# Performance work log

Measured on AMD Instinct MI355X. Metric: run time of the kernel, lower is better.

## Reference

```python
import jax, jax.numpy as jnp
import numpy as np

N_NODES = 50000
N_EDGES = 800000
IN_CH, HID_CH, OUT_CH = 128, 256, 128


def _glorot(key, shape):
    fan_in, fan_out = shape[1], shape[0]
    lim = float(np.sqrt(6.0 / (fan_in + fan_out)))
    return jax.random.uniform(key, shape, jnp.float32, -lim, lim)


def setup_inputs() -> dict:
    key = jax.random.key(0)
    ks = jax.random.split(key, 8)
    x = jax.random.normal(ks[0], (N_NODES, IN_CH), jnp.float32)
    edge_index = jax.random.randint(ks[1], (2, N_EDGES), 0, N_NODES, jnp.int64)
    return {
        "x": x,
        "edge_index": edge_index,
        # layer 1: SAGEConv(128 -> 256): lin_l (with bias) on aggregated, lin_r (no bias) on root
        "W1l": _glorot(ks[2], (HID_CH, IN_CH)),
        "b1l": jnp.zeros((HID_CH,), jnp.float32),
        "W1r": _glorot(ks[3], (HID_CH, IN_CH)),
        # layer 2: SAGEConv(256 -> 128)
        "W2l": _glorot(ks[4], (OUT_CH, HID_CH)),
        "b2l": jnp.zeros((OUT_CH,), jnp.float32),
        "W2r": _glorot(ks[5], (OUT_CH, HID_CH)),
    }


def _sage_conv(x, src, dst, Wl, bl, Wr, n_nodes):
    # mean-aggregate neighbor (source) features at destination nodes
    msg = x[src]                                                   # [E, C] gather
    agg = jax.ops.segment_sum(msg, dst, num_segments=n_nodes)      # [N, C]
    deg = jax.ops.segment_sum(jnp.ones((src.shape[0],), x.dtype), dst,
                              num_segments=n_nodes)                # [N]
    mean = agg / jnp.maximum(deg, 1.0)[:, None]                    # zero-degree -> 0
    return mean @ Wl.T + bl + x @ Wr.T


def reference(x, edge_index, W1l, b1l, W1r, W2l, b2l, W2r):
    src, dst = edge_index[0], edge_index[1]
    n = x.shape[0]
    h = _sage_conv(x, src, dst, W1l, b1l, W1r, n)
    h = jax.nn.relu(h)  # dropout is identity in eval mode
    out = _sage_conv(h, src, dst, W2l, b2l, W2r, n)
    return out
```

## Files before the change

kernel.cpp:

```cpp
#include <hip/hip_runtime.h>

#define N_NODES 50000
#define IN_CH   128
#define HID_CH  256
#define OUT_CH  128

#define NB    196
#define NWG   64
#define NBNW  (NB * NWG)
#define SCHUNK 49

#define XBLK  3125
#define WBLK  64

typedef __attribute__((ext_vector_type(8))) short bf16x8;
typedef __attribute__((ext_vector_type(4))) float f32x4;
typedef __attribute__((ext_vector_type(2))) float f32x2;

__device__ __forceinline__ unsigned short f32_bf16_rne(float f) {
    unsigned u = __float_as_uint(f);
    unsigned r = u + 0x7fff + ((u >> 16) & 1);
    return (unsigned short)(r >> 16);
}

__device__ __forceinline__ void cvt8(const float* __restrict__ in,
                                     unsigned short* __restrict__ outp, size_t j)
{
    const float4* p = reinterpret_cast<const float4*>(in) + 2 * j;
    float4 a = p[0], b = p[1];
    alignas(16) unsigned short t[8] = {
        f32_bf16_rne(a.x), f32_bf16_rne(a.y), f32_bf16_rne(a.z), f32_bf16_rne(a.w),
        f32_bf16_rne(b.x), f32_bf16_rne(b.y), f32_bf16_rne(b.z), f32_bf16_rne(b.w)};
    *reinterpret_cast<int4*>(outp + 8 * j) = *reinterpret_cast<const int4*>(t);
}

__global__ __launch_bounds__(256) void prep_kernel(
    const int* __restrict__ src, const int* __restrict__ dst,
    int* __restrict__ counts, int E, int chunk,
    const float* __restrict__ x, unsigned short* __restrict__ xb,
    unsigned char* __restrict__ xb8,
    const float* __restrict__ W1l, const float* __restrict__ W1r,
    const float* __restrict__ W2l, const float* __restrict__ W2r,
    unsigned short* __restrict__ W1lb, unsigned short* __restrict__ W1rb,
    unsigned short* __restrict__ W2lb, unsigned short* __restrict__ W2rb)
{
    const int b = blockIdx.x;
    if (b < NWG) {
        __shared__ int h[NB];
        for (int i = threadIdx.x; i < NB; i += 256) h[i] = 0;
        __syncthreads();
        const int e0 = b * chunk;
        const int e1 = min(e0 + chunk, E);
        for (int e = e0 + threadIdx.x; e < e1; e += 256) {
            int s = src[e], d = dst[e];
            if ((unsigned)s < (unsigned)N_NODES && (unsigned)d < (unsigned)N_NODES)
                atomicAdd(&h[d >> 8], 1);
        }
        __syncthreads();
        for (int i = threadIdx.x; i < NB; i += 256)
            counts[i * NWG + b] = h[i];
    } else if (b < NWG + XBLK) {
        size_t j = (size_t)(b - NWG) * 256 + threadIdx.x;
        const float4* p = reinterpret_cast<const float4*>(x) + 2 * j;
        float4 a = p[0], bb = p[1];
        alignas(16) unsigned short t[8] = {
            f32_bf16_rne(a.x),  f32_bf16_rne(a.y),  f32_bf16_rne(a.z),  f32_bf16_rne(a.w),
            f32_bf16_rne(bb.x), f32_bf16_rne(bb.y), f32_bf16_rne(bb.z), f32_bf16_rne(bb.w)};
        *reinterpret_cast<int4*>(xb + 8 * j) = *reinterpret_cast<const int4*>(t);
        unsigned u0 = __builtin_amdgcn_cvt_pk_fp8_f32(a.x, a.y, 0, false);
        u0 = __builtin_amdgcn_cvt_pk_fp8_f32(a.z, a.w, u0, true);
        unsigned u1 = __builtin_amdgcn_cvt_pk_fp8_f32(bb.x, bb.y, 0, false);
        u1 = __builtin_amdgcn_cvt_pk_fp8_f32(bb.z, bb.w, u1, true);
        uint2 uv; uv.x = u0; uv.y = u1;
        *reinterpret_cast<uint2*>(xb8 + 8 * j) = uv;
    } else {
        int idx = (b - NWG - XBLK) * 256 + threadIdx.x;
        int seg = idx >> 12, j = idx & 4095;
        const float* in = (seg == 0) ? W1l : (seg == 1) ? W1r : (seg == 2) ? W2l : W2r;
        unsigned short* o = (seg == 0) ? W1lb : (seg == 1) ? W1rb : (seg == 2) ? W2lb : W2rb;
        cvt8(in, o, (size_t)j);
    }
}

__global__ __launch_bounds__(256) void scan_all_kernel(
    const int* __restrict__ counts, int* __restrict__ S)
{
    __shared__ int tot[256];
    const int t = threadIdx.x;
    const int base = t * SCHUNK;
    int loc[SCHUNK];
    int sum = 0;
#pragma unroll
    for (int k = 0; k < SCHUNK; ++k) {
        loc[k] = sum;
        sum += counts[base + k];
    }
    tot[t] = sum;
    __syncthreads();
    for (int off = 1; off < 256; off <<= 1) {
        int v = (t >= off) ? tot[t - off] : 0;
        __syncthreads();
        if (t >= off) tot[t] += v;
        __syncthreads();
    }
    int offv = (t == 0) ? 0 : tot[t - 1];
#pragma unroll
    for (int k = 0; k < SCHUNK; ++k)
        S[base + k] = loc[k] + offv;
    if (t == 255) S[NBNW] = offv + sum;
}

__global__ __launch_bounds__(256) void bscatter_kernel(
    const int* __restrict__ src, const int* __restrict__ dst,
    const int* __restrict__ S, int* __restrict__ pairs, int E, int chunk)
{
    __shared__ int cur[NB];
    const int w = blockIdx.x;
    for (int i = threadIdx.x; i < NB; i += 256) cur[i] = S[i * NWG + w];
    __syncthreads();
    const int e0 = w * chunk;
    const int e1 = min(e0 + chunk, E);
    for (int e = e0 + threadIdx.x; e < e1; e += 256) {
        int s = src[e], d = dst[e];
        if ((unsigned)s < (unsigned)N_NODES && (unsigned)d < (unsigned)N_NODES) {
            int pos = atomicAdd(&cur[d >> 8], 1);
            pairs[pos] = (s << 8) | (d & 255);
        }
    }
}

__global__ __launch_bounds__(256) void bsort_kernel(
    const int* __restrict__ pairs, const int* __restrict__ S,
    int* __restrict__ rowptr, int* __restrict__ colidx)
{
    __shared__ int hcnt[256];
    __shared__ int hcur[256];
    const int b = blockIdx.x;
    const int start = S[b * NWG];
    const int endv  = (b == NB - 1) ? S[NBNW] : S[(b + 1) * NWG];

    hcnt[threadIdx.x] = 0;
    __syncthreads();
    for (int e = start + threadIdx.x; e < endv; e += 256)
        atomicAdd(&hcnt[pairs[e] & 255], 1);
    __syncthreads();
    for (int off = 1; off < 256; off <<= 1) {
        int t = (threadIdx.x >= off) ? hcnt[threadIdx.x - off] : 0;
        __syncthreads();
        if (threadIdx.x >= off) hcnt[threadIdx.x] += t;
        __syncthreads();
    }
    int offv = (threadIdx.x == 0) ? 0 : hcnt[threadIdx.x - 1];
    hcur[threadIdx.x] = offv;
    int node = (b << 8) + threadIdx.x;
    if (node < N_NODES) rowptr[node] = start + offv;
    if (b == NB - 1 && threadIdx.x == 0) rowptr[N_NODES] = endv;
    __syncthreads();
    for (int e = start + threadIdx.x; e < endv; e += 256) {
        int p = pairs[e];
        int pos = atomicAdd(&hcur[p & 255], 1);
        colidx[start + pos] = (unsigned)p >> 8;
    }
}

#define ACC8(v)                                                              \
    { f32x2 t0 = __builtin_amdgcn_cvt_pk_f32_fp8(v.x, false);                \
      f32x2 t1 = __builtin_amdgcn_cvt_pk_f32_fp8(v.x, true);                 \
      f32x2 t2 = __builtin_amdgcn_cvt_pk_f32_fp8(v.y, false);                \
      f32x2 t3 = __builtin_amdgcn_cvt_pk_f32_fp8(v.y, true);                 \
      acc[0] += t0.x; acc[1] += t0.y; acc[2] += t1.x; acc[3] += t1.y;        \
      acc[4] += t2.x; acc[5] += t2.y; acc[6] += t3.x; acc[7] += t3.y; }

#define AGG_BODY(CH)                                                            \
    const int node = blockIdx.x * 16 + (threadIdx.x >> 4);                      \
    if (node >= N_NODES) return;                                                \
    const int l8 = threadIdx.x & 15;                                            \
    const int beg = rowptr[node], end = rowptr[node + 1];                       \
    const int len = end - beg;                                                  \
    float acc[8] = {};                                                          \
    for (int base = beg; base < end; base += 16) {                              \
        const int cnt = min(16, end - base);                                    \
        int ci = colidx[base + ((l8 < cnt) ? l8 : 0)];                          \
        int k = 0;                                                              \
        for (; k + 3 < cnt; k += 4) {                                           \
            int s0 = __shfl(ci, k, 16),     s1 = __shfl(ci, k + 1, 16);         \
            int s2 = __shfl(ci, k + 2, 16), s3 = __shfl(ci, k + 3, 16);         \
            uint2 v0 = *reinterpret_cast<const uint2*>(feat + (size_t)s0 * CH + l8 * 8); \
            uint2 v1 = *reinterpret_cast<const uint2*>(feat + (size_t)s1 * CH + l8 * 8); \
            uint2 v2 = *reinterpret_cast<const uint2*>(feat + (size_t)s2 * CH + l8 * 8); \
            uint2 v3 = *reinterpret_cast<const uint2*>(feat + (size_t)s3 * CH + l8 * 8); \
            ACC8(v0) ACC8(v1) ACC8(v2) ACC8(v3)                                 \
        }                                                                       \
        for (; k < cnt; ++k) {                                                  \
            int s0 = __shfl(ci, k, 16);                                         \
            uint2 v0 = *reinterpret_cast<const uint2*>(feat + (size_t)s0 * CH + l8 * 8); \
            ACC8(v0)                                                            \
        }                                                                       \
    }                                                                           \
    const float sc = 1.0f / fmaxf((float)len, 1.0f);

__global__ __launch_bounds__(256) void agg1_kernel(
    const unsigned char* __restrict__ feat, const int* __restrict__ rowptr,
    const int* __restrict__ colidx, unsigned short* __restrict__ outp)
{
    AGG_BODY(IN_CH)
    alignas(16) unsigned short t[8];
#pragma unroll
    for (int k = 0; k < 8; ++k) t[k] = f32_bf16_rne(acc[k] * sc);
    *reinterpret_cast<int4*>(outp + (size_t)node * IN_CH + l8 * 8) =
        *reinterpret_cast<const int4*>(t);
}

__global__ __launch_bounds__(256) void agg2_kernel(
    const unsigned char* __restrict__ feat, const int* __restrict__ rowptr,
    const int* __restrict__ colidx, float* __restrict__ out)
{
    AGG_BODY(OUT_CH)
    float* o = out + (size_t)node * OUT_CH + l8 * 8;
    float4 o0 = reinterpret_cast<float4*>(o)[0];
    float4 o1 = reinterpret_cast<float4*>(o)[1];
    o0.x += acc[0] * sc; o0.y += acc[1] * sc; o0.z += acc[2] * sc; o0.w += acc[3] * sc;
    o1.x += acc[4] * sc; o1.y += acc[5] * sc; o1.z += acc[6] * sc; o1.w += acc[7] * sc;
    reinterpret_cast<float4*>(o)[0] = o0;
    reinterpret_cast<float4*>(o)[1] = o1;
}

__device__ __forceinline__ void stage_async(
    const unsigned short* __restrict__ g, int ldg, int rowBase, int maxRow,
    int kBase, unsigned short* __restrict__ s, int tid)
{
    const int wave = tid >> 6;
    const int lane = tid & 63;
    const int r_in = lane >> 3;
    const int c_g  = (lane & 7) ^ r_in;
#pragma unroll
    for (int it = 0; it < 4; ++it) {
        const int rowBlk = it * 32 + wave * 8;
        int row = rowBase + rowBlk + r_in;
        if (row >= maxRow) row = maxRow - 1;
        const unsigned short* gp = g + (size_t)row * ldg + kBase + c_g * 8;
        unsigned short* lp = s + rowBlk * 64;
        __builtin_amdgcn_global_load_lds(
            (const __attribute__((address_space(1))) unsigned int*)gp,
            (__attribute__((address_space(3))) unsigned int*)lp,
            16, 0, 0);
    }
}

__device__ __forceinline__ const bf16x8* frag_ptr(
    const unsigned short* __restrict__ s, int rr, int c)
{
    return reinterpret_cast<const bf16x8*>(s + rr * 64 + (((c ^ (rr & 7))) << 3));
}

__device__ __forceinline__ void mfma_tile(
    const unsigned short* __restrict__ As, const unsigned short* __restrict__ Bs,
    int wm, int wn, int l16, int quad, f32x4 acc[4][4])
{
#pragma unroll
    for (int k0 = 0; k0 < 64; k0 += 32) {
        const int c = (k0 >> 3) + quad;
        bf16x8 a[4], b[4];
#pragma unroll
        for (int i = 0; i < 4; ++i)
            a[i] = *frag_ptr(As, wm * 64 + i * 16 + l16, c);
#pragma unroll
        for (int j = 0; j < 4; ++j)
            b[j] = *frag_ptr(Bs, wn * 64 + j * 16 + l16, c);
#pragma unroll
        for (int i = 0; i < 4; ++i)
#pragma unroll
            for (int j = 0; j < 4; ++j)
                acc[i][j] = __builtin_amdgcn_mfma_f32_16x16x32_bf16(
                    b[j], a[i], acc[i][j], 0, 0, 0);
    }
}

__global__ __launch_bounds__(256) void gemm1_mfma(
    const unsigned short* __restrict__ mean1b, const unsigned short* __restrict__ xb,
    const unsigned short* __restrict__ W1lb,   const unsigned short* __restrict__ W1rb,
    const float* __restrict__ b1l, unsigned short* __restrict__ hb)
{
    __shared__ unsigned short As[128 * 64];
    __shared__ unsigned short Bs[128 * 64];
    const int tid = threadIdx.x;
    const int wid = tid >> 6, lane = tid & 63;
    const int wm = wid & 1, wn = wid >> 1;
    const int l16 = lane & 15, quad = lane >> 4;
    const int rowBase = blockIdx.x * 128;
    const int colBase = blockIdx.y * 128;

    f32x4 z = {0.f, 0.f, 0.f, 0.f};
    f32x4 acc[4][4];
#pragma unroll
    for (int i = 0; i < 4; ++i)
#pragma unroll
        for (int j = 0; j < 4; ++j) acc[i][j] = z;

#pragma unroll
    for (int op = 0; op < 2; ++op) {
        const unsigned short* A = op ? xb : mean1b;
        const unsigned short* B = op ? W1rb : W1lb;
#pragma unroll
        for (int kb = 0; kb < IN_CH; kb += 64) {
            __syncthreads();
            stage_async(A, IN_CH, rowBase, N_NODES, kb, As, tid);
            stage_async(B, IN_CH, colBase, HID_CH, kb, Bs, tid);
            __syncthreads();
            mfma_tile(As, Bs, wm, wn, l16, quad, acc);
        }
    }

#pragma unroll
    for (int i = 0; i < 4; ++i) {
        int m = rowBase + wm * 64 + i * 16 + l16;
        if (m >= N_NODES) continue;
#pragma unroll
        for (int j = 0; j < 4; ++j) {
            int col = colBase + wn * 64 + j * 16 + quad * 4;
            float4 bv = *reinterpret_cast<const float4*>(b1l + col);
            alignas(8) unsigned short t[4];
            t[0] = f32_bf16_rne(fmaxf(acc[i][j][0] + bv.x, 0.0f));
            t[1] = f32_bf16_rne(fmaxf(acc[i][j][1] + bv.y, 0.0f));
            t[2] = f32_bf16_rne(fmaxf(acc[i][j][2] + bv.z, 0.0f));
            t[3] = f32_bf16_rne(fmaxf(acc[i][j][3] + bv.w, 0.0f));
            *reinterpret_cast<uint2*>(hb + (size_t)m * HID_CH + col) =
                *reinterpret_cast<const uint2*>(t);
        }
    }
}

__global__ __launch_bounds__(256) void gemm2_mfma(
    const unsigned short* __restrict__ hb, const unsigned short* __restrict__ W2lb,
    const unsigned short* __restrict__ W2rb, const float* __restrict__ b2l,
    unsigned char* __restrict__ pb8, float* __restrict__ out)
{
    __shared__ unsigned short As[128 * 64];
    __shared__ unsigned short Bs[128 * 64];
    const int tid = threadIdx.x;
    const int wid = tid >> 6, lane = tid & 63;
    const int wm = wid & 1, wn = wid >> 1;
    const int l16 = lane & 15, quad = lane >> 4;
    const int rowBase = blockIdx.x * 128;
    const unsigned short* B = blockIdx.y ? W2rb : W2lb;

    f32x4 z = {0.f, 0.f, 0.f, 0.f};
    f32x4 acc[4][4];
#pragma unroll
    for (int i = 0; i < 4; ++i)
#pragma unroll
        for (int j = 0; j < 4; ++j) acc[i][j] = z;

#pragma unroll
    for (int kb = 0; kb < HID_CH; kb += 64) {
        __syncthreads();
        stage_async(hb, HID_CH, rowBase, N_NODES, kb, As, tid);
        stage_async(B, HID_CH, 0, OUT_CH, kb, Bs, tid);
        __syncthreads();
        mfma_tile(As, Bs, wm, wn, l16, quad, acc);
    }

    if (blockIdx.y == 0) {
#pragma unroll
        for (int i = 0; i < 4; ++i) {
            int m = rowBase + wm * 64 + i * 16 + l16;
            if (m >= N_NODES) continue;
#pragma unroll
            for (int j = 0; j < 4; ++j) {
                int col = wn * 64 + j * 16 + quad * 4;
                unsigned u = __builtin_amdgcn_cvt_pk_fp8_f32(
                    acc[i][j][0], acc[i][j][1], 0, false);
                u = __builtin_amdgcn_cvt_pk_fp8_f32(
                    acc[i][j][2], acc[i][j][3], u, true);
                *reinterpret_cast<unsigned*>(pb8 + (size_t)m * OUT_CH + col) = u;
            }
        }
    } else {
#pragma unroll
        for (int i = 0; i < 4; ++i) {
            int m = rowBase + wm * 64 + i * 16 + l16;
            if (m >= N_NODES) continue;
#pragma unroll
            for (int j = 0; j < 4; ++j) {
                int col = wn * 64 + j * 16 + quad * 4;
                float4 bv = *reinterpret_cast<const float4*>(b2l + col);
                float4 o;
                o.x = acc[i][j][0] + bv.x;
                o.y = acc[i][j][1] + bv.y;
                o.z = acc[i][j][2] + bv.z;
                o.w = acc[i][j][3] + bv.w;
                *reinterpret_cast<float4*>(out + (size_t)m * OUT_CH + col) = o;
            }
        }
    }
}

extern "C" void kernel_launch(void* const* d_in, const int* in_sizes, int n_in,
                              void* d_out, int out_size, void* d_ws, size_t ws_size,
                              hipStream_t stream)
{
    const float* x   = (const float*)d_in[0];
    const int*   ei  = (const int*)d_in[1];
    const float* W1l = (const float*)d_in[2];
    const float* b1l = (const float*)d_in[3];
    const float* W1r = (const float*)d_in[4];
    const float* W2l = (const float*)d_in[5];
    const float* b2l = (const float*)d_in[6];
    const float* W2r = (const float*)d_in[7];

    const int E = in_sizes[1] / 2;
    const int* src = ei;
    const int* dst = ei + E;

    char* ws = (char*)d_ws;
    size_t off = 0;
    auto alloc = [&](size_t bytes) {
        void* p = ws + off;
        off += (bytes + 255) & ~(size_t)255;
        return p;
    };
    unsigned short* xb     = (unsigned short*)alloc((size_t)N_NODES * IN_CH * 2);
    unsigned char*  xb8    = (unsigned char*)alloc((size_t)N_NODES * IN_CH);
    unsigned short* mean1b = (unsigned short*)alloc((size_t)N_NODES * IN_CH * 2);
    unsigned short* hb     = (unsigned short*)alloc((size_t)N_NODES * HID_CH * 2);
    unsigned char*  pb8    = (unsigned char*)alloc((size_t)N_NODES * OUT_CH);
    unsigned short* W1lb   = (unsigned short*)alloc((size_t)HID_CH * IN_CH * 2);
    unsigned short* W1rb   = (unsigned short*)alloc((size_t)HID_CH * IN_CH * 2);
    unsigned short* W2lb   = (unsigned short*)alloc((size_t)OUT_CH * HID_CH * 2);
    unsigned short* W2rb   = (unsigned short*)alloc((size_t)OUT_CH * HID_CH * 2);
    int* counts = (int*)alloc((size_t)NBNW * 4);
    int* S      = (int*)alloc((size_t)(NBNW + 1) * 4);
    int* pairs  = (int*)alloc((size_t)E * 4);
    int* rowptr = (int*)alloc((size_t)(N_NODES + 1) * 4);
    int* colidx = (int*)alloc((size_t)E * 4);
    float* out = (float*)d_out;

    const int chunk = (E + NWG - 1) / NWG;

    prep_kernel<<<NWG + XBLK + WBLK, 256, 0, stream>>>(
        src, dst, counts, E, chunk, x, xb, xb8,
        W1l, W1r, W2l, W2r, W1lb, W1rb, W2lb, W2rb);
    scan_all_kernel<<<1, 256, 0, stream>>>(counts, S);
    bscatter_kernel<<<NWG, 256, 0, stream>>>(src, dst, S, pairs, E, chunk);
    bsort_kernel<<<NB, 256, 0, stream>>>(pairs, S, rowptr, colidx);

    const int aggBlocks = (N_NODES + 15) / 16;
    const int mBlocks = (N_NODES + 127) / 128;

    agg1_kernel<<<aggBlocks, 256, 0, stream>>>(xb8, rowptr, colidx, mean1b);
    gemm1_mfma<<<dim3(mBlocks, HID_CH / 128), 256, 0, stream>>>(
        mean1b, xb, W1lb, W1rb, b1l, hb);
    gemm2_mfma<<<dim3(mBlocks, 2), 256, 0, stream>>>(hb, W2lb, W2rb, b2l, pb8, out);
    agg2_kernel<<<aggBlocks, 256, 0, stream>>>(pb8, rowptr, colidx, out);
}
```

Baseline: 219.6 us.

## Parallelize bucket scan, unroll gather by 8, store layer-2 root term as bf16

The bucket counts grid grows from 64 to 256 workgroups, and the single-block scan becomes a multi-block scan in which each block reduces all earlier counts itself. This spreads the bucketing and scan work across more of the GPU, at the cost of redundant prefix reductions. The aggregation inner loop now issues 8 independent gathers at a time for more memory-level parallelism. gemm2 writes its root-term output as bf16 instead of fp32 with bias, and agg2 adds the bias itself, which halves that intermediate's traffic but adds bf16 rounding error to the final output.

```diff
diff --git a/kernel.cpp b/kernel.cpp
--- a/kernel.cpp
+++ b/kernel.cpp
@@ -6,9 +6,8 @@
 #define OUT_CH  128
 
 #define NB    196
-#define NWG   64
+#define NWG   256
 #define NBNW  (NB * NWG)
-#define SCHUNK 49
 
 #define XBLK  3125
 #define WBLK  64
@@ -82,32 +81,34 @@
     }
 }
 
-__global__ __launch_bounds__(256) void scan_all_kernel(
+__global__ __launch_bounds__(256) void scan_kernel(
     const int* __restrict__ counts, int* __restrict__ S)
 {
-    __shared__ int tot[256];
+    __shared__ int red[256];
     const int t = threadIdx.x;
-    const int base = t * SCHUNK;
-    int loc[SCHUNK];
-    int sum = 0;
-#pragma unroll
-    for (int k = 0; k < SCHUNK; ++k) {
-        loc[k] = sum;
-        sum += counts[base + k];
-    }
-    tot[t] = sum;
+    const int b = blockIdx.x;
+    const int lim = b * NWG;
+    int partial = 0;
+    for (int i = t; i < lim; i += 256) partial += counts[i];
+    red[t] = partial;
+    __syncthreads();
+    for (int off = 128; off >= 1; off >>= 1) {
+        if (t < off) red[t] += red[t + off];
+        __syncthreads();
+    }
+    const int base_b = red[0];
+    __syncthreads();
+    const int v = counts[b * NWG + t];
+    red[t] = v;
     __syncthreads();
     for (int off = 1; off < 256; off <<= 1) {
-        int v = (t >= off) ? tot[t - off] : 0;
-        __syncthreads();
-        if (t >= off) tot[t] += v;
-        __syncthreads();
-    }
-    int offv = (t == 0) ? 0 : tot[t - 1];
-#pragma unroll
-    for (int k = 0; k < SCHUNK; ++k)
-        S[base + k] = loc[k] + offv;
-    if (t == 255) S[NBNW] = offv + sum;
+        int u = (t >= off) ? red[t - off] : 0;
+        __syncthreads();
+        if (t >= off) red[t] += u;
+        __syncthreads();
+    }
+    S[b * NWG + t] = base_b + red[t] - v;
+    if (b == NB - 1 && t == 255) S[NBNW] = base_b + red[255];
 }
 
 __global__ __launch_bounds__(256) void bscatter_kernel(
@@ -170,6 +171,8 @@
       f32x2 t3 = __builtin_amdgcn_cvt_pk_f32_fp8(v.y, true);                 \
       acc[0] += t0.x; acc[1] += t0.y; acc[2] += t1.x; acc[3] += t1.y;        \
       acc[4] += t2.x; acc[5] += t2.y; acc[6] += t3.x; acc[7] += t3.y; }
+
+#define LDROW(s, CH) (*reinterpret_cast<const uint2*>(feat + (size_t)(s) * (CH) + l8 * 8))
 
 #define AGG_BODY(CH)                                                            \
     const int node = blockIdx.x * 16 + (threadIdx.x >> 4);                      \
@@ -182,18 +185,28 @@
         const int cnt = min(16, end - base);                                    \
         int ci = colidx[base + ((l8 < cnt) ? l8 : 0)];                          \
         int k = 0;                                                              \
+        for (; k + 7 < cnt; k += 8) {                                           \
+            int s0 = __shfl(ci, k, 16),     s1 = __shfl(ci, k + 1, 16);         \
+            int s2 = __shfl(ci, k + 2, 16), s3 = __shfl(ci, k + 3, 16);         \
+            int s4 = __shfl(ci, k + 4, 16), s5 = __shfl(ci, k + 5, 16);         \
+            int s6 = __shfl(ci, k + 6, 16), s7 = __shfl(ci, k + 7, 16);         \
+            uint2 v0 = LDROW(s0, CH); uint2 v1 = LDROW(s1, CH);                 \
+            uint2 v2 = LDROW(s2, CH); uint2 v3 = LDROW(s3, CH);                 \
+            uint2 v4 = LDROW(s4, CH); uint2 v5 = LDROW(s5, CH);                 \
+            uint2 v6 = LDROW(s6, CH); uint2 v7 = LDROW(s7, CH);                 \
+            ACC8(v0) ACC8(v1) ACC8(v2) ACC8(v3)                                 \
+            ACC8(v4) ACC8(v5) ACC8(v6) ACC8(v7)                                 \
+        }                                                                       \
         for (; k + 3 < cnt; k += 4) {                                           \
             int s0 = __shfl(ci, k, 16),     s1 = __shfl(ci, k + 1, 16);         \
             int s2 = __shfl(ci, k + 2, 16), s3 = __shfl(ci, k + 3, 16);         \
-            uint2 v0 = *reinterpret_cast<const uint2*>(feat + (size_t)s0 * CH + l8 * 8); \
-            uint2 v1 = *reinterpret_cast<const uint2*>(feat + (size_t)s1 * CH + l8 * 8); \
-            uint2 v2 = *reinterpret_cast<const uint2*>(feat + (size_t)s2 * CH + l8 * 8); \
-            uint2 v3 = *reinterpret_cast<const uint2*>(feat + (size_t)s3 * CH + l8 * 8); \
+            uint2 v0 = LDROW(s0, CH); uint2 v1 = LDROW(s1, CH);                 \
+            uint2 v2 = LDROW(s2, CH); uint2 v3 = LDROW(s3, CH);                 \
             ACC8(v0) ACC8(v1) ACC8(v2) ACC8(v3)                                 \
         }                                                                       \
         for (; k < cnt; ++k) {                                                  \
             int s0 = __shfl(ci, k, 16);                                         \
-            uint2 v0 = *reinterpret_cast<const uint2*>(feat + (size_t)s0 * CH + l8 * 8); \
+            uint2 v0 = LDROW(s0, CH);                                           \
             ACC8(v0)                                                            \
         }                                                                       \
     }                                                                           \
@@ -213,14 +226,24 @@
 
 __global__ __launch_bounds__(256) void agg2_kernel(
     const unsigned char* __restrict__ feat, const int* __restrict__ rowptr,
-    const int* __restrict__ colidx, float* __restrict__ out)
+    const int* __restrict__ colidx, const unsigned short* __restrict__ hrb,
+    const float* __restrict__ b2l, float* __restrict__ out)
 {
     AGG_BODY(OUT_CH)
+    const int4 hv = *reinterpret_cast<const int4*>(hrb + (size_t)node * OUT_CH + l8 * 8);
+    const unsigned short* hs = reinterpret_cast<const unsigned short*>(&hv);
+    float4 b0 = *reinterpret_cast<const float4*>(b2l + l8 * 8);
+    float4 b1 = *reinterpret_cast<const float4*>(b2l + l8 * 8 + 4);
+    float4 o0, o1;
+    o0.x = acc[0] * sc + __uint_as_float((unsigned)hs[0] << 16) + b0.x;
+    o0.y = acc[1] * sc + __uint_as_float((unsigned)hs[1] << 16) + b0.y;
+    o0.z = acc[2] * sc + __uint_as_float((unsigned)hs[2] << 16) + b0.z;
+    o0.w = acc[3] * sc + __uint_as_float((unsigned)hs[3] << 16) + b0.w;
+    o1.x = acc[4] * sc + __uint_as_float((unsigned)hs[4] << 16) + b1.x;
+    o1.y = acc[5] * sc + __uint_as_float((unsigned)hs[5] << 16) + b1.y;
+    o1.z = acc[6] * sc + __uint_as_float((unsigned)hs[6] << 16) + b1.z;
+    o1.w = acc[7] * sc + __uint_as_float((unsigned)hs[7] << 16) + b1.w;
     float* o = out + (size_t)node * OUT_CH + l8 * 8;
-    float4 o0 = reinterpret_cast<float4*>(o)[0];
-    float4 o1 = reinterpret_cast<float4*>(o)[1];
-    o0.x += acc[0] * sc; o0.y += acc[1] * sc; o0.z += acc[2] * sc; o0.w += acc[3] * sc;
-    o1.x += acc[4] * sc; o1.y += acc[5] * sc; o1.z += acc[6] * sc; o1.w += acc[7] * sc;
     reinterpret_cast<float4*>(o)[0] = o0;
     reinterpret_cast<float4*>(o)[1] = o1;
 }
@@ -332,8 +355,8 @@
 
 __global__ __launch_bounds__(256) void gemm2_mfma(
     const unsigned short* __restrict__ hb, const unsigned short* __restrict__ W2lb,
-    const unsigned short* __restrict__ W2rb, const float* __restrict__ b2l,
-    unsigned char* __restrict__ pb8, float* __restrict__ out)
+    const unsigned short* __restrict__ W2rb,
+    unsigned char* __restrict__ pb8, unsigned short* __restrict__ hrb)
 {
     __shared__ unsigned short As[128 * 64];
     __shared__ unsigned short Bs[128 * 64];
@@ -383,13 +406,13 @@
 #pragma unroll
             for (int j = 0; j < 4; ++j) {
                 int col = wn * 64 + j * 16 + quad * 4;
-                float4 bv = *reinterpret_cast<const float4*>(b2l + col);
-                float4 o;
-                o.x = acc[i][j][0] + bv.x;
-                o.y = acc[i][j][1] + bv.y;
-                o.z = acc[i][j][2] + bv.z;
-                o.w = acc[i][j][3] + bv.w;
-                *reinterpret_cast<float4*>(out + (size_t)m * OUT_CH + col) = o;
+                alignas(8) unsigned short t[4];
+                t[0] = f32_bf16_rne(acc[i][j][0]);
+                t[1] = f32_bf16_rne(acc[i][j][1]);
+                t[2] = f32_bf16_rne(acc[i][j][2]);
+                t[3] = f32_bf16_rne(acc[i][j][3]);
+                *reinterpret_cast<uint2*>(hrb + (size_t)m * OUT_CH + col) =
+                    *reinterpret_cast<const uint2*>(t);
             }
         }
     }
@@ -424,6 +447,7 @@
     unsigned short* mean1b = (unsigned short*)alloc((size_t)N_NODES * IN_CH * 2);
     unsigned short* hb     = (unsigned short*)alloc((size_t)N_NODES * HID_CH * 2);
     unsigned char*  pb8    = (unsigned char*)alloc((size_t)N_NODES * OUT_CH);
+    unsigned short* hrb    = (unsigned short*)alloc((size_t)N_NODES * OUT_CH * 2);
     unsigned short* W1lb   = (unsigned short*)alloc((size_t)HID_CH * IN_CH * 2);
     unsigned short* W1rb   = (unsigned short*)alloc((size_t)HID_CH * IN_CH * 2);
     unsigned short* W2lb   = (unsigned short*)alloc((size_t)OUT_CH * HID_CH * 2);
@@ -440,7 +464,7 @@
     prep_kernel<<<NWG + XBLK + WBLK, 256, 0, stream>>>(
         src, dst, counts, E, chunk, x, xb, xb8,
         W1l, W1r, W2l, W2r, W1lb, W1rb, W2lb, W2rb);
-    scan_all_kernel<<<1, 256, 0, stream>>>(counts, S);
+    scan_kernel<<<NB, 256, 0, stream>>>(counts, S);
     bscatter_kernel<<<NWG, 256, 0, stream>>>(src, dst, S, pairs, E, chunk);
     bsort_kernel<<<NB, 256, 0, stream>>>(pairs, S, rowptr, colidx);
 
@@ -450,6 +474,6 @@
     agg1_kernel<<<aggBlocks, 256, 0, stream>>>(xb8, rowptr, colidx, mean1b);
     gemm1_mfma<<<dim3(mBlocks, HID_CH / 128), 256, 0, stream>>>(
         mean1b, xb, W1lb, W1rb, b1l, hb);
-    gemm2_mfma<<<dim3(mBlocks, 2), 256, 0, stream>>>(hb, W2lb, W2rb, b2l, pb8, out);
-    agg2_kernel<<<aggBlocks, 256, 0, stream>>>(pb8, rowptr, colidx, out);
-}
+    gemm2_mfma<<<dim3(mBlocks, 2), 256, 0, stream>>>(hb, W2lb, W2rb, pb8, hrb);
+    agg2_kernel<<<aggBlocks, 256, 0, stream>>>(pb8, rowptr, colidx, hrb, b2l, out);
+}
```

Measured after the change: 223.7 us. Within noise of the previous version (+1.9%).
